# Kernel optimization log

Measured on AMD Instinct MI355X. Metric: run time of the kernel, lower is better.

The kernel has to match this reference:

```python
import jax, jax.numpy as jnp
import numpy as np

D_MODEL = 512
N_HEADS = 8
D_K = D_MODEL // N_HEADS


def setup_inputs() -> dict:
    key = jax.random.key(0)
    kq, kk, kv = jax.random.split(key, 3)
    shape = (4, 2048, D_MODEL)
    return {
        "Q": jax.random.normal(kq, shape, dtype=jnp.float32),
        "K": jax.random.normal(kk, shape, dtype=jnp.float32),
        "V": jax.random.normal(kv, shape, dtype=jnp.float32),
    }


def reference(Q, K, V):
    B, S, _ = Q.shape
    # [B, S, H, Dk] -> [B, H, S, Dk]
    q = Q.reshape(B, S, N_HEADS, D_K).transpose(0, 2, 1, 3)
    k = K.reshape(B, S, N_HEADS, D_K).transpose(0, 2, 1, 3)
    v = V.reshape(B, S, N_HEADS, D_K).transpose(0, 2, 1, 3)
    scale = 1.0 / (D_K ** 0.5)
    # [B, H, S, S] scores (faithful to original: full matrix materialized)
    scores = jnp.einsum("bhqd,bhkd->bhqk", q, k) * scale
    attn = jax.nn.softmax(scores, axis=-1)
    out = jnp.einsum("bhqk,bhkd->bhqd", attn, v)
    # [B, H, S, Dk] -> [B, S, D_MODEL]
    return out.transpose(0, 2, 1, 3).reshape(B, S, D_MODEL)
```

## Files before the change

### kernel.cpp

```cpp
#include <hip/hip_runtime.h>
#include <hip/hip_bf16.h>

#define SEQ    2048
#define DMODEL 512
#define NH     8
#define QBLK   256
#define KVB    128
#define NT2    (SEQ / KVB)

#if __has_builtin(__builtin_amdgcn_exp2f)
#define EXPFN(x) __builtin_amdgcn_exp2f(x)
#define QSCALE 0.18033688011112042f
#else
#define EXPFN(x) __expf(x)
#define QSCALE 0.125f
#endif

typedef __attribute__((ext_vector_type(8)))  short     bf16x8;
typedef __attribute__((ext_vector_type(16))) float     f32x16;
typedef __attribute__((ext_vector_type(2)))  int       i32x2;

#define MFMA32(A, B, C) __builtin_amdgcn_mfma_f32_32x32x16_bf16(A, B, C, 0, 0, 0)

__device__ __forceinline__ unsigned short f2bf(float f) {
  union { float f; unsigned u; } x; x.f = f;
  return (unsigned short)((x.u + 0x7FFFu + ((x.u >> 16) & 1u)) >> 16);
}

__device__ __forceinline__ int cvtpk(float lo, float hi) {
  int r;
  asm("v_cvt_pk_bf16_f32 %0, %1, %2" : "=v"(r) : "v"(lo), "v"(hi));
  return r;
}

__device__ __forceinline__ i32x2 plswap(int a, int b) {
#if __has_builtin(__builtin_amdgcn_permlane32_swap)
  return __builtin_amdgcn_permlane32_swap(a, b, false, false);
#else
  int a2 = __shfl_xor(a, 32), b2 = __shfl_xor(b, 32);
  int hi = (threadIdx.x >> 5) & 1;
  i32x2 r; r.x = hi ? b2 : a; r.y = hi ? b : a2; return r;
#endif
}

__device__ __forceinline__ void gload16(const void* g, void* l) {
  __builtin_amdgcn_global_load_lds(
      (const __attribute__((address_space(1))) void*)g,
      (__attribute__((address_space(3))) void*)l, 16, 0, 0);
}

__global__ void prep_kv(const float* __restrict__ K, const float* __restrict__ V,
                        unsigned short* __restrict__ kb, unsigned short* __restrict__ vb) {
  if (blockIdx.x < 2048) {
    int gid = blockIdx.x * 256 + threadIdx.x;
    int g  = gid & 7;
    int s  = (gid >> 3) & (SEQ - 1);
    int bh = gid >> 14;
    int b = bh >> 3, h = bh & 7;
    const float* src = K + ((size_t)(b * SEQ + s) * DMODEL) + h * 64 + (g << 3);
    float4 a = ((const float4*)src)[0];
    float4 c = ((const float4*)src)[1];
    bf16x8 w;
    w[0] = (short)f2bf(a.x); w[1] = (short)f2bf(a.y);
    w[2] = (short)f2bf(a.z); w[3] = (short)f2bf(a.w);
    w[4] = (short)f2bf(c.x); w[5] = (short)f2bf(c.y);
    w[6] = (short)f2bf(c.z); w[7] = (short)f2bf(c.w);
    int r = s & 63;
    int slot = ((((r >> 5) << 3) + g) ^ (r & 15));
    unsigned short* dst = kb + ((size_t)bh * SEQ + (s & ~63)) * 64
                             + ((r & 31) << 7) + (slot << 3);
    *(bf16x8*)dst = w;
  } else {
    int bt = blockIdx.x - 2048;
    int bh = bt >> 5, tile = bt & 31;
    int b = bh >> 3, h = bh & 7;
    int t  = threadIdx.x;
    int d  = t & 63;
    int kg = t >> 6;
    const float* src = V + ((size_t)(b * SEQ + tile * 64 + kg * 16) * DMODEL) + h * 64 + d;
    float v[16];
#pragma unroll
    for (int j = 0; j < 16; ++j) v[j] = src[(size_t)j * DMODEL];
    bf16x8 lo, hi8;
#pragma unroll
    for (int j = 0; j < 8; ++j) { lo[j] = (short)f2bf(v[j]); hi8[j] = (short)f2bf(v[8 + j]); }
    unsigned short* base = vb + ((size_t)bt << 12);
    int g0 = kg << 1, g1 = (kg << 1) | 1;
    int rb = (((d >> 5) << 3));
    int s0 = ((rb + g0) ^ (d & 15));
    int s1 = ((rb + g1) ^ (d & 15));
    unsigned short* row = base + ((d & 31) << 7);
    *(bf16x8*)(row + (s0 << 3)) = lo;
    *(bf16x8*)(row + (s1 << 3)) = hi8;
  }
}

__global__ __launch_bounds__(512, 2)
void fa_fwd(const float* __restrict__ Q, const unsigned short* __restrict__ Kb,
            const unsigned short* __restrict__ Vb, float* __restrict__ O) {
  __shared__ unsigned short kt[2][KVB * 64];
  __shared__ unsigned short vt[2][64 * KVB];

  const int tid = threadIdx.x;
  const int wv  = tid >> 6;
  const int ln  = tid & 63;
  const int l31 = ln & 31;
  const int hi  = ln >> 5;

  const int orig = blockIdx.x;
  const int wgid = (orig & 7) * 32 + (orig >> 3);
  const int bh = wgid >> 3;
  const int qt = wgid & 7;
  const int b = bh >> 3, h = bh & 7;

  const float* Qh = Q + (size_t)b * SEQ * DMODEL + (size_t)h * 64;
  float*       Oh = O + (size_t)b * SEQ * DMODEL + (size_t)h * 64;
  const unsigned short* Kh = Kb + (size_t)bh * SEQ * 64;
  const unsigned short* Vh = Vb + (size_t)bh * SEQ * 64;

  const int q = qt * QBLK + wv * 32 + l31;

  bf16x8 qf[4];
  {
    const float* qp = Qh + (size_t)q * DMODEL + (hi << 3);
#pragma unroll
    for (int t = 0; t < 4; ++t) {
      float4 a = *(const float4*)(qp + 16 * t);
      float4 c = *(const float4*)(qp + 16 * t + 4);
      bf16x8 w;
      w[0] = (short)f2bf(a.x * QSCALE); w[1] = (short)f2bf(a.y * QSCALE);
      w[2] = (short)f2bf(a.z * QSCALE); w[3] = (short)f2bf(a.w * QSCALE);
      w[4] = (short)f2bf(c.x * QSCALE); w[5] = (short)f2bf(c.y * QSCALE);
      w[6] = (short)f2bf(c.z * QSCALE); w[7] = (short)f2bf(c.w * QSCALE);
      qf[t] = w;
    }
  }

  const int rowb = l31 << 7;
  int ca[4], cb[4];
#pragma unroll
  for (int t = 0; t < 4; ++t) {
    int g = 2 * t + hi;
    ca[t] = rowb + (((g)     ^ (l31 & 15)) << 3);
    cb[t] = rowb + (((8 + g) ^ (l31 & 15)) << 3);
  }

  f32x16 o0 = {}, o1 = {};
  float l = 0.f;

#define STAGE(T2, B)                                                       \
  do {                                                                     \
    const char* gk = (const char*)(Kh + (size_t)(T2) * KVB * 64);          \
    const char* gv = (const char*)(Vh + (size_t)(T2) * KVB * 64);          \
    char* lk = (char*)&kt[(B)][0];                                         \
    char* lv = (char*)&vt[(B)][0];                                         \
    gload16(gk + (((wv)     * 64 + ln) << 4), lk + ((wv)     << 10));      \
    gload16(gk + (((wv + 8) * 64 + ln) << 4), lk + ((wv + 8) << 10));      \
    gload16(gv + (((wv)     * 64 + ln) << 4), lv + ((wv)     << 10));      \
    gload16(gv + (((wv + 8) * 64 + ln) << 4), lv + ((wv + 8) << 10));      \
  } while (0)

  auto qk64 = [&](const unsigned short* ktb, int base, f32x16& s0, f32x16& s1) {
    f32x16 u0 = {}, u1 = {};
#pragma unroll
    for (int ks = 0; ks < 4; ++ks) {
      bf16x8 k0 = *(const bf16x8*)&ktb[base + ca[ks]];
      bf16x8 k1 = *(const bf16x8*)&ktb[base + cb[ks]];
      __builtin_amdgcn_s_setprio(1);
      u0 = MFMA32(k0, qf[ks], u0);
      u1 = MFMA32(k1, qf[ks], u1);
      __builtin_amdgcn_s_setprio(0);
    }
    s0 = u0; s1 = u1;
  };

  auto smpv64 = [&](f32x16& s0, f32x16& s1, const unsigned short* vtb, int base) {
#pragma unroll
    for (int ks = 0; ks < 4; ++ks) {
      float e[8];
#pragma unroll
      for (int j = 0; j < 8; ++j) {
        float sv = (ks < 2) ? s0[(ks & 1) * 8 + j] : s1[(ks & 1) * 8 + j];
        e[j] = EXPFN(sv);
      }
      l += ((e[0] + e[1]) + (e[2] + e[3])) + ((e[4] + e[5]) + (e[6] + e[7]));
      i32x2 r0 = plswap(cvtpk(e[0], e[1]), cvtpk(e[4], e[5]));
      i32x2 r1 = plswap(cvtpk(e[2], e[3]), cvtpk(e[6], e[7]));
      union { int i[4]; bf16x8 v; } pa;
      pa.i[0] = r0.x; pa.i[1] = r1.x; pa.i[2] = r0.y; pa.i[3] = r1.y;

      bf16x8 v0 = *(const bf16x8*)&vtb[base + ca[ks]];
      bf16x8 v1 = *(const bf16x8*)&vtb[base + cb[ks]];
      __builtin_amdgcn_s_setprio(1);
      o0 = MFMA32(v0, pa.v, o0);
      o1 = MFMA32(v1, pa.v, o1);
      __builtin_amdgcn_s_setprio(0);
    }
  };

  auto tilec = [&](const unsigned short* ktb, const unsigned short* vtb) {
    f32x16 sA0, sA1, sB0, sB1;
    qk64(ktb, 0,    sA0, sA1);
    qk64(ktb, 4096, sB0, sB1);
    smpv64(sA0, sA1, vtb, 0);
    smpv64(sB0, sB1, vtb, 4096);
  };

  STAGE(0, 0);
  __syncthreads();
  for (int t = 0; t < NT2; t += 2) {
    STAGE(t + 1, 1);
    tilec(kt[0], vt[0]);
    __syncthreads();
    if (t + 2 < NT2) STAGE(t + 2, 0);
    tilec(kt[1], vt[1]);
    __syncthreads();
  }

  l += __shfl_xor(l, 32);
  float rinv = 1.0f / l;
  float* op = Oh + (size_t)q * DMODEL;
#pragma unroll
  for (int r4 = 0; r4 < 4; ++r4) {
    float4 w0, w1;
    w0.x = o0[4 * r4 + 0] * rinv; w0.y = o0[4 * r4 + 1] * rinv;
    w0.z = o0[4 * r4 + 2] * rinv; w0.w = o0[4 * r4 + 3] * rinv;
    w1.x = o1[4 * r4 + 0] * rinv; w1.y = o1[4 * r4 + 1] * rinv;
    w1.z = o1[4 * r4 + 2] * rinv; w1.w = o1[4 * r4 + 3] * rinv;
    *(float4*)(op + 8 * r4 + 4 * hi)      = w0;
    *(float4*)(op + 32 + 8 * r4 + 4 * hi) = w1;
  }
}

extern "C" void kernel_launch(void* const* d_in, const int* in_sizes, int n_in,
                              void* d_out, int out_size, void* d_ws, size_t ws_size,
                              hipStream_t stream) {
  const float* Q = (const float*)d_in[0];
  const float* K = (const float*)d_in[1];
  const float* V = (const float*)d_in[2];
  float* O = (float*)d_out;
  unsigned short* kb = (unsigned short*)d_ws;
  unsigned short* vb = kb + (size_t)32 * SEQ * 64;
  prep_kv<<<3072, 256, 0, stream>>>(K, V, kb, vb);
  fa_fwd<<<256, 512, 0, stream>>>(Q, kb, vb, O);
}
```

Measured before the change: 55.72 us.

## Split KV range in halves with 64-query waves and add combine kernel

The main attention kernel now splits each head's key range into two halves. Each wave handles 64 queries (two 32-row MFMA groups), so every K/V fragment read from LDS feeds twice as many MFMAs. Partial outputs are written as fp16 along with fp32 row sums, and a new combine kernel merges the two halves into the final fp32 output. The cost is an extra launch, extra global traffic for the fp16 partials, fp16 rounding of intermediate outputs, and occupancy lowered to one block per CU. The old single-pass kernel stays as a fallback when the workspace is too small.

```diff
diff --git a/kernel.cpp b/kernel.cpp
--- a/kernel.cpp
+++ b/kernel.cpp
@@ -1,12 +1,15 @@
 #include <hip/hip_runtime.h>
 #include <hip/hip_bf16.h>
+#include <hip/hip_fp16.h>
 
 #define SEQ    2048
 #define DMODEL 512
 #define NH     8
-#define QBLK   256
 #define KVB    128
-#define NT2    (SEQ / KVB)
+#define QW     64
+#define QBLK   512
+#define HKEYS  (SEQ / 2)
+#define NINT   (HKEYS / KVB)
 
 #if __has_builtin(__builtin_amdgcn_exp2f)
 #define EXPFN(x) __builtin_amdgcn_exp2f(x)
@@ -19,6 +22,8 @@
 typedef __attribute__((ext_vector_type(8)))  short     bf16x8;
 typedef __attribute__((ext_vector_type(16))) float     f32x16;
 typedef __attribute__((ext_vector_type(2)))  int       i32x2;
+typedef __attribute__((ext_vector_type(4)))  _Float16  f16x4;
+typedef __attribute__((ext_vector_type(8)))  _Float16  f16x8;
 
 #define MFMA32(A, B, C) __builtin_amdgcn_mfma_f32_32x32x16_bf16(A, B, C, 0, 0, 0)
 
@@ -95,9 +100,10 @@
   }
 }
 
-__global__ __launch_bounds__(512, 2)
-void fa_fwd(const float* __restrict__ Q, const unsigned short* __restrict__ Kb,
-            const unsigned short* __restrict__ Vb, float* __restrict__ O) {
+__global__ __launch_bounds__(512, 1)
+void fa_fwd_split(const float* __restrict__ Q, const unsigned short* __restrict__ Kb,
+                  const unsigned short* __restrict__ Vb,
+                  _Float16* __restrict__ opart, float* __restrict__ lsum) {
   __shared__ unsigned short kt[2][KVB * 64];
   __shared__ unsigned short vt[2][64 * KVB];
 
@@ -109,30 +115,37 @@
 
   const int orig = blockIdx.x;
   const int wgid = (orig & 7) * 32 + (orig >> 3);
-  const int bh = wgid >> 3;
-  const int qt = wgid & 7;
+  const int bh   = wgid >> 3;
+  const int qt   = (wgid >> 1) & 3;
+  const int half = wgid & 1;
   const int b = bh >> 3, h = bh & 7;
 
   const float* Qh = Q + (size_t)b * SEQ * DMODEL + (size_t)h * 64;
-  float*       Oh = O + (size_t)b * SEQ * DMODEL + (size_t)h * 64;
-  const unsigned short* Kh = Kb + (size_t)bh * SEQ * 64;
-  const unsigned short* Vh = Vb + (size_t)bh * SEQ * 64;
-
-  const int q = qt * QBLK + wv * 32 + l31;
-
-  bf16x8 qf[4];
+  const unsigned short* Kh = Kb + (size_t)bh * SEQ * 64 + (size_t)half * HKEYS * 64;
+  const unsigned short* Vh = Vb + (size_t)bh * SEQ * 64 + (size_t)half * HKEYS * 64;
+
+  const int qA = qt * QBLK + wv * QW + l31;
+
+  bf16x8 qfA[4], qfB[4];
   {
-    const float* qp = Qh + (size_t)q * DMODEL + (hi << 3);
+    const float* qpA = Qh + (size_t)qA * DMODEL + (hi << 3);
+    const float* qpB = qpA + 32 * DMODEL;
 #pragma unroll
     for (int t = 0; t < 4; ++t) {
-      float4 a = *(const float4*)(qp + 16 * t);
-      float4 c = *(const float4*)(qp + 16 * t + 4);
-      bf16x8 w;
-      w[0] = (short)f2bf(a.x * QSCALE); w[1] = (short)f2bf(a.y * QSCALE);
-      w[2] = (short)f2bf(a.z * QSCALE); w[3] = (short)f2bf(a.w * QSCALE);
-      w[4] = (short)f2bf(c.x * QSCALE); w[5] = (short)f2bf(c.y * QSCALE);
-      w[6] = (short)f2bf(c.z * QSCALE); w[7] = (short)f2bf(c.w * QSCALE);
-      qf[t] = w;
+      float4 a0 = *(const float4*)(qpA + 16 * t);
+      float4 a1 = *(const float4*)(qpA + 16 * t + 4);
+      float4 b0 = *(const float4*)(qpB + 16 * t);
+      float4 b1 = *(const float4*)(qpB + 16 * t + 4);
+      bf16x8 wa, wb;
+      wa[0] = (short)f2bf(a0.x * QSCALE); wa[1] = (short)f2bf(a0.y * QSCALE);
+      wa[2] = (short)f2bf(a0.z * QSCALE); wa[3] = (short)f2bf(a0.w * QSCALE);
+      wa[4] = (short)f2bf(a1.x * QSCALE); wa[5] = (short)f2bf(a1.y * QSCALE);
+      wa[6] = (short)f2bf(a1.z * QSCALE); wa[7] = (short)f2bf(a1.w * QSCALE);
+      wb[0] = (short)f2bf(b0.x * QSCALE); wb[1] = (short)f2bf(b0.y * QSCALE);
+      wb[2] = (short)f2bf(b0.z * QSCALE); wb[3] = (short)f2bf(b0.w * QSCALE);
+      wb[4] = (short)f2bf(b1.x * QSCALE); wb[5] = (short)f2bf(b1.y * QSCALE);
+      wb[6] = (short)f2bf(b1.z * QSCALE); wb[7] = (short)f2bf(b1.w * QSCALE);
+      qfA[t] = wa; qfB[t] = wb;
     }
   }
 
@@ -145,8 +158,8 @@
     cb[t] = rowb + (((8 + g) ^ (l31 & 15)) << 3);
   }
 
-  f32x16 o0 = {}, o1 = {};
-  float l = 0.f;
+  f32x16 oA0 = {}, oA1 = {}, oB0 = {}, oB1 = {};
+  float lA = 0.f, lB = 0.f;
 
 #define STAGE(T2, B)                                                       \
   do {                                                                     \
@@ -160,6 +173,191 @@
     gload16(gv + (((wv + 8) * 64 + ln) << 4), lv + ((wv + 8) << 10));      \
   } while (0)
 
+  auto sub64 = [&](const unsigned short* ktb, const unsigned short* vtb, int base) {
+    f32x16 sA0 = {}, sA1 = {}, sB0 = {}, sB1 = {};
+#pragma unroll
+    for (int ks = 0; ks < 4; ++ks) {
+      bf16x8 k0 = *(const bf16x8*)&ktb[base + ca[ks]];
+      bf16x8 k1 = *(const bf16x8*)&ktb[base + cb[ks]];
+      __builtin_amdgcn_s_setprio(1);
+      sA0 = MFMA32(k0, qfA[ks], sA0);
+      sB0 = MFMA32(k0, qfB[ks], sB0);
+      sA1 = MFMA32(k1, qfA[ks], sA1);
+      sB1 = MFMA32(k1, qfB[ks], sB1);
+      __builtin_amdgcn_s_setprio(0);
+    }
+#pragma unroll
+    for (int ks = 0; ks < 4; ++ks) {
+      float eA[8], eB[8];
+#pragma unroll
+      for (int j = 0; j < 8; ++j) {
+        float svA = (ks < 2) ? sA0[(ks & 1) * 8 + j] : sA1[(ks & 1) * 8 + j];
+        float svB = (ks < 2) ? sB0[(ks & 1) * 8 + j] : sB1[(ks & 1) * 8 + j];
+        eA[j] = EXPFN(svA);
+        eB[j] = EXPFN(svB);
+      }
+      lA += ((eA[0] + eA[1]) + (eA[2] + eA[3])) + ((eA[4] + eA[5]) + (eA[6] + eA[7]));
+      lB += ((eB[0] + eB[1]) + (eB[2] + eB[3])) + ((eB[4] + eB[5]) + (eB[6] + eB[7]));
+      i32x2 ra0 = plswap(cvtpk(eA[0], eA[1]), cvtpk(eA[4], eA[5]));
+      i32x2 ra1 = plswap(cvtpk(eA[2], eA[3]), cvtpk(eA[6], eA[7]));
+      i32x2 rb0 = plswap(cvtpk(eB[0], eB[1]), cvtpk(eB[4], eB[5]));
+      i32x2 rb1 = plswap(cvtpk(eB[2], eB[3]), cvtpk(eB[6], eB[7]));
+      union { int i[4]; bf16x8 v; } paA, paB;
+      paA.i[0] = ra0.x; paA.i[1] = ra1.x; paA.i[2] = ra0.y; paA.i[3] = ra1.y;
+      paB.i[0] = rb0.x; paB.i[1] = rb1.x; paB.i[2] = rb0.y; paB.i[3] = rb1.y;
+
+      bf16x8 v0 = *(const bf16x8*)&vtb[base + ca[ks]];
+      bf16x8 v1 = *(const bf16x8*)&vtb[base + cb[ks]];
+      __builtin_amdgcn_s_setprio(1);
+      oA0 = MFMA32(v0, paA.v, oA0);
+      oB0 = MFMA32(v0, paB.v, oB0);
+      oA1 = MFMA32(v1, paA.v, oA1);
+      oB1 = MFMA32(v1, paB.v, oB1);
+      __builtin_amdgcn_s_setprio(0);
+    }
+  };
+
+  auto tilec = [&](const unsigned short* ktb, const unsigned short* vtb) {
+    sub64(ktb, vtb, 0);
+    sub64(ktb, vtb, 4096);
+  };
+
+  STAGE(0, 0);
+  __syncthreads();
+  for (int t = 0; t < NINT; t += 2) {
+    STAGE(t + 1, 1);
+    tilec(kt[0], vt[0]);
+    __syncthreads();
+    if (t + 2 < NINT) STAGE(t + 2, 0);
+    tilec(kt[1], vt[1]);
+    __syncthreads();
+  }
+
+  lA += __shfl_xor(lA, 32);
+  lB += __shfl_xor(lB, 32);
+  float riA = 1.0f / lA;
+  float riB = 1.0f / lB;
+  const size_t rowA = (size_t)bh * SEQ + qA;
+  if (hi == 0) {
+    lsum[(size_t)half * 32 * SEQ + rowA]      = lA;
+    lsum[(size_t)half * 32 * SEQ + rowA + 32] = lB;
+  }
+  _Float16* opA = opart + (size_t)half * 32 * SEQ * 64 + rowA * 64;
+  _Float16* opB = opA + 32 * 64;
+#pragma unroll
+  for (int r4 = 0; r4 < 4; ++r4) {
+    f16x4 wa0, wa1, wb0, wb1;
+#pragma unroll
+    for (int j = 0; j < 4; ++j) {
+      wa0[j] = (_Float16)(oA0[4 * r4 + j] * riA);
+      wa1[j] = (_Float16)(oA1[4 * r4 + j] * riA);
+      wb0[j] = (_Float16)(oB0[4 * r4 + j] * riB);
+      wb1[j] = (_Float16)(oB1[4 * r4 + j] * riB);
+    }
+    *(f16x4*)(opA + 8 * r4 + 4 * hi)      = wa0;
+    *(f16x4*)(opA + 32 + 8 * r4 + 4 * hi) = wa1;
+    *(f16x4*)(opB + 8 * r4 + 4 * hi)      = wb0;
+    *(f16x4*)(opB + 32 + 8 * r4 + 4 * hi) = wb1;
+  }
+}
+
+__global__ __launch_bounds__(256)
+void fa_combine(const _Float16* __restrict__ opart, const float* __restrict__ lsum,
+                float* __restrict__ O) {
+  int idx  = blockIdx.x * 256 + threadIdx.x;
+  int dg   = idx & 7;
+  int qrow = (idx >> 3) & (SEQ - 1);
+  int bh   = idx >> 14;
+  size_t row = (size_t)bh * SEQ + qrow;
+
+  float l1 = lsum[row];
+  float l2 = lsum[(size_t)32 * SEQ + row];
+  float w  = 1.0f / (l1 + l2);
+  float w1 = l1 * w, w2 = l2 * w;
+
+  f16x8 h1 = *(const f16x8*)(opart + row * 64 + dg * 8);
+  f16x8 h2 = *(const f16x8*)(opart + (size_t)32 * SEQ * 64 + row * 64 + dg * 8);
+
+  int b = bh >> 3, h = bh & 7;
+  float* out = O + ((size_t)(b * SEQ + qrow)) * DMODEL + h * 64 + dg * 8;
+  float4 v0, v1;
+  v0.x = w1 * (float)h1[0] + w2 * (float)h2[0];
+  v0.y = w1 * (float)h1[1] + w2 * (float)h2[1];
+  v0.z = w1 * (float)h1[2] + w2 * (float)h2[2];
+  v0.w = w1 * (float)h1[3] + w2 * (float)h2[3];
+  v1.x = w1 * (float)h1[4] + w2 * (float)h2[4];
+  v1.y = w1 * (float)h1[5] + w2 * (float)h2[5];
+  v1.z = w1 * (float)h1[6] + w2 * (float)h2[6];
+  v1.w = w1 * (float)h1[7] + w2 * (float)h2[7];
+  ((float4*)out)[0] = v0;
+  ((float4*)out)[1] = v1;
+}
+
+__global__ __launch_bounds__(512, 2)
+void fa_fwd(const float* __restrict__ Q, const unsigned short* __restrict__ Kb,
+            const unsigned short* __restrict__ Vb, float* __restrict__ O) {
+  __shared__ unsigned short kt[2][KVB * 64];
+  __shared__ unsigned short vt[2][64 * KVB];
+
+  const int tid = threadIdx.x;
+  const int wv  = tid >> 6;
+  const int ln  = tid & 63;
+  const int l31 = ln & 31;
+  const int hi  = ln >> 5;
+
+  const int orig = blockIdx.x;
+  const int wgid = (orig & 7) * 32 + (orig >> 3);
+  const int bh = wgid >> 3;
+  const int qt = wgid & 7;
+  const int b = bh >> 3, h = bh & 7;
+
+  const float* Qh = Q + (size_t)b * SEQ * DMODEL + (size_t)h * 64;
+  float*       Oh = O + (size_t)b * SEQ * DMODEL + (size_t)h * 64;
+  const unsigned short* Kh = Kb + (size_t)bh * SEQ * 64;
+  const unsigned short* Vh = Vb + (size_t)bh * SEQ * 64;
+
+  const int q = qt * 256 + wv * 32 + l31;
+
+  bf16x8 qf[4];
+  {
+    const float* qp = Qh + (size_t)q * DMODEL + (hi << 3);
+#pragma unroll
+    for (int t = 0; t < 4; ++t) {
+      float4 a = *(const float4*)(qp + 16 * t);
+      float4 c = *(const float4*)(qp + 16 * t + 4);
+      bf16x8 w;
+      w[0] = (short)f2bf(a.x * QSCALE); w[1] = (short)f2bf(a.y * QSCALE);
+      w[2] = (short)f2bf(a.z * QSCALE); w[3] = (short)f2bf(a.w * QSCALE);
+      w[4] = (short)f2bf(c.x * QSCALE); w[5] = (short)f2bf(c.y * QSCALE);
+      w[6] = (short)f2bf(c.z * QSCALE); w[7] = (short)f2bf(c.w * QSCALE);
+      qf[t] = w;
+    }
+  }
+
+  const int rowb = l31 << 7;
+  int ca[4], cb[4];
+#pragma unroll
+  for (int t = 0; t < 4; ++t) {
+    int g = 2 * t + hi;
+    ca[t] = rowb + (((g)     ^ (l31 & 15)) << 3);
+    cb[t] = rowb + (((8 + g) ^ (l31 & 15)) << 3);
+  }
+
+  f32x16 o0 = {}, o1 = {};
+  float l = 0.f;
+
+#define STAGEF(T2, B)                                                      \
+  do {                                                                     \
+    const char* gk = (const char*)(Kh + (size_t)(T2) * KVB * 64);          \
+    const char* gv = (const char*)(Vh + (size_t)(T2) * KVB * 64);          \
+    char* lk = (char*)&kt[(B)][0];                                         \
+    char* lv = (char*)&vt[(B)][0];                                         \
+    gload16(gk + (((wv)     * 64 + ln) << 4), lk + ((wv)     << 10));      \
+    gload16(gk + (((wv + 8) * 64 + ln) << 4), lk + ((wv + 8) << 10));      \
+    gload16(gv + (((wv)     * 64 + ln) << 4), lv + ((wv)     << 10));      \
+    gload16(gv + (((wv + 8) * 64 + ln) << 4), lv + ((wv + 8) << 10));      \
+  } while (0)
+
   auto qk64 = [&](const unsigned short* ktb, int base, f32x16& s0, f32x16& s1) {
     f32x16 u0 = {}, u1 = {};
 #pragma unroll
@@ -206,13 +404,13 @@
     smpv64(sB0, sB1, vtb, 4096);
   };
 
-  STAGE(0, 0);
+  STAGEF(0, 0);
   __syncthreads();
-  for (int t = 0; t < NT2; t += 2) {
-    STAGE(t + 1, 1);
+  for (int t = 0; t < SEQ / KVB; t += 2) {
+    STAGEF(t + 1, 1);
     tilec(kt[0], vt[0]);
     __syncthreads();
-    if (t + 2 < NT2) STAGE(t + 2, 0);
+    if (t + 2 < SEQ / KVB) STAGEF(t + 2, 0);
     tilec(kt[1], vt[1]);
     __syncthreads();
   }
@@ -239,8 +437,21 @@
   const float* K = (const float*)d_in[1];
   const float* V = (const float*)d_in[2];
   float* O = (float*)d_out;
+
   unsigned short* kb = (unsigned short*)d_ws;
   unsigned short* vb = kb + (size_t)32 * SEQ * 64;
   prep_kv<<<3072, 256, 0, stream>>>(K, V, kb, vb);
-  fa_fwd<<<256, 512, 0, stream>>>(Q, kb, vb, O);
-}
+
+  const size_t base   = (size_t)2 * 32 * SEQ * 64 * sizeof(unsigned short);
+  const size_t needsp = base + (size_t)2 * 32 * SEQ * 64 * sizeof(_Float16)
+                              + (size_t)2 * 32 * SEQ * sizeof(float);
+  if (ws_size >= needsp + (1u << 20)) {
+    _Float16* opart = (_Float16*)((char*)d_ws + base);
+    float*    ls    = (float*)((char*)d_ws + base +
+                       (size_t)2 * 32 * SEQ * 64 * sizeof(_Float16));
+    fa_fwd_split<<<256, 512, 0, stream>>>(Q, kb, vb, opart, ls);
+    fa_combine<<<2048, 256, 0, stream>>>(opart, ls, O);
+  } else {
+    fa_fwd<<<256, 512, 0, stream>>>(Q, kb, vb, O);
+  }
+}
```

New measurement: 73.64 us. +32.2%, slower.
